# Kernel tuning notes

Hardware: AMD Instinct MI355X
Metric: run time of the kernel (lower is better)

Reference implementation:

```python
import jax, jax.numpy as jnp
import numpy as np

B, T = 32768, 32
OBJ_V, PRED_V = 179, 46
E_OBJ, E_PRED, H = 5, 5, 32
IN_DIM = E_OBJ + E_PRED + 2 + 4  # 16, matches LSTMCell input size


def setup_inputs() -> dict:
    key = jax.random.key(0)
    ks = jax.random.split(key, 12)
    s = 0.1
    return {
        "input_objects": jax.random.randint(ks[0], (B, T), 0, OBJ_V),
        "input_boxes": jax.random.uniform(ks[1], (B, T, 4), dtype=jnp.float32),
        "predicates": jax.random.randint(ks[2], (B, T), 0, PRED_V),
        "subject_indicators": jax.random.randint(ks[3], (B, T), 0, 2),
        "target_object": jax.random.randint(ks[4], (B,), 0, OBJ_V),
        "obj_emb": jax.random.normal(ks[5], (OBJ_V, E_OBJ), dtype=jnp.float32) * s,
        "pred_emb": jax.random.normal(ks[6], (PRED_V, E_PRED), dtype=jnp.float32) * s,
        "W_ih": jax.random.normal(ks[7], (4 * H, IN_DIM), dtype=jnp.float32) * s,
        "W_hh": jax.random.normal(ks[8], (4 * H, H), dtype=jnp.float32) * s,
        "b_ih": jnp.zeros((4 * H,), dtype=jnp.float32),
        "b_hh": jnp.zeros((4 * H,), dtype=jnp.float32),
        "fc2_W": jax.random.normal(ks[9], (4, H), dtype=jnp.float32) * s,
        "fc2_b": jnp.zeros((4,), dtype=jnp.float32),
    }


def _forward(input_objects, input_boxes, predicates, subject_indicators,
             obj_emb, pred_emb, W_ih, W_hh, b_ih, b_hh, fc2_W, fc2_b):
    # concatenate_features, vectorized over all timesteps at once: [B,T,16]
    feats = jnp.concatenate([
        obj_emb[input_objects],                                   # [B,T,5]
        pred_emb[predicates],                                     # [B,T,5]
        jax.nn.one_hot(subject_indicators, 2, dtype=jnp.float32), # [B,T,2]
        input_boxes,                                              # [B,T,4]
    ], axis=-1)
    xs = jnp.transpose(feats, (1, 0, 2))  # [T,B,16] for scan over time

    def step(carry, x):
        h, c = carry
        gates = x @ W_ih.T + b_ih + h @ W_hh.T + b_hh  # [B,4H]
        i, f, g, o = jnp.split(gates, 4, axis=-1)      # torch gate order i,f,g,o
        i = jax.nn.sigmoid(i)
        f = jax.nn.sigmoid(f)
        g = jnp.tanh(g)
        o = jax.nn.sigmoid(o)
        c = f * c + i * g
        h = o * jnp.tanh(c)
        return (h, c), None

    h0 = jnp.zeros((input_objects.shape[0], H), dtype=jnp.float32)
    (h, _), _ = jax.lax.scan(step, (h0, h0), xs)
    out = h @ fc2_W.T + fc2_b          # output_fc2 on last hidden state
    return jnp.clip(out, 0.0, 1.0)     # torch.clamp(min=0, max=1)


def reference(input_objects, input_boxes, predicates, subject_indicators, target_object,
              obj_emb, pred_emb, W_ih, W_hh, b_ih, b_hh, fc2_W, fc2_b):
    # target_object is accepted by the torch forward but unused in its body
    return _forward(input_objects, input_boxes, predicates, subject_indicators,
                    obj_emb, pred_emb, W_ih, W_hh, b_ih, b_hh, fc2_W, fc2_b)
```

## Files before the change

kernel.cpp:

```cpp
#include <hip/hip_runtime.h>

#define LDS_BYTES 16672

typedef _Float16 f16x8 __attribute__((ext_vector_type(8)));
typedef float    f32x4 __attribute__((ext_vector_type(4)));

#define LOG2E     1.44269504088896f
#define TWO_LOG2E 2.88539008177793f

__device__ __forceinline__ float sig_pre(float a) {
    return __builtin_amdgcn_rcpf(1.0f + __builtin_amdgcn_exp2f(a));
}
__device__ __forceinline__ float tanh_pre(float a) {
    return 1.0f - 2.0f * __builtin_amdgcn_rcpf(1.0f + __builtin_amdgcn_exp2f(a));
}
__device__ __forceinline__ int pack2(float a, float b) {
    union { _Float16 h[2]; int i; } u;
    u.h[0] = (_Float16)a; u.h[1] = (_Float16)b;
    return u.i;
}

__global__ __launch_bounds__(64, 2)
void lstm_fused(const int* __restrict__ objs,
                const float* __restrict__ boxes,
                const int* __restrict__ preds,
                const int* __restrict__ subj,
                const float* __restrict__ obj_emb,
                const float* __restrict__ pred_emb,
                const float* __restrict__ W_ih,
                const float* __restrict__ W_hh,
                const float* __restrict__ b_ih,
                const float* __restrict__ b_hh,
                const float* __restrict__ fc2_W,
                const float* __restrict__ fc2_b,
                float* __restrict__ out)
{
    extern __shared__ char smem[];
    const int tid  = threadIdx.x;
    const int quad = tid >> 4;
    const int cidx = tid & 15;
    const int XOFF = 0, ZOFF = 16640;

    if (tid < 8) ((int*)(smem + ZOFF))[tid] = 0;

    {
        int b  = tid >> 2;
        int t0 = (tid & 3) << 3;
        long gb = (long)blockIdx.x * 16 + b;
        const int* op = objs  + gb * 32 + t0;
        const int* pp = preds + gb * 32 + t0;
        const int* sp = subj  + gb * 32 + t0;
        #pragma unroll
        for (int c = 0; c < 8; c += 4) {
            int4 ov = *(const int4*)(op + c);
            int4 pv = *(const int4*)(pp + c);
            int4 sv = *(const int4*)(sp + c);
            int oarr[4] = {ov.x, ov.y, ov.z, ov.w};
            int parr[4] = {pv.x, pv.y, pv.z, pv.w};
            int sarr[4] = {sv.x, sv.y, sv.z, sv.w};
            #pragma unroll
            for (int tt = 0; tt < 4; ++tt) {
                int t = t0 + c + tt;
                const float* eo = obj_emb  + oarr[tt] * 5;
                const float* ep = pred_emb + parr[tt] * 5;
                float4 bx = *(const float4*)(boxes + (gb * 32 + t) * 4);
                f16x8 lo, hi;
                lo[0]=(_Float16)eo[0]; lo[1]=(_Float16)eo[1]; lo[2]=(_Float16)eo[2];
                lo[3]=(_Float16)eo[3]; lo[4]=(_Float16)eo[4];
                lo[5]=(_Float16)ep[0]; lo[6]=(_Float16)ep[1]; lo[7]=(_Float16)ep[2];
                hi[0]=(_Float16)ep[3]; hi[1]=(_Float16)ep[4];
                hi[2]=(_Float16)(sarr[tt]==0 ? 1.0f : 0.0f);
                hi[3]=(_Float16)(sarr[tt]==1 ? 1.0f : 0.0f);
                hi[4]=(_Float16)bx.x; hi[5]=(_Float16)bx.y;
                hi[6]=(_Float16)bx.z; hi[7]=(_Float16)bx.w;
                char* dst = smem + XOFF + b * 1040 + t * 32;
                *(f16x8*)dst        = lo;
                *(f16x8*)(dst + 16) = hi;
            }
        }
    }

    f16x8 Wf[8][2];
    f32x4 bias4[8];
    #pragma unroll
    for (int j = 0; j < 8; ++j) {
        int g = j >> 1, half = j & 1;
        float scale = (g == 2) ? TWO_LOG2E : -LOG2E;
        int um = 8 * (cidx >> 2) + (cidx & 3) + 4 * half;
        int n  = g * 32 + um;
        #pragma unroll
        for (int ks = 0; ks < 2; ++ks) {
            f16x8 v;
            #pragma unroll
            for (int jj = 0; jj < 8; ++jj) {
                int k = ks * 32 + quad * 8 + jj;
                float val = (k < 16) ? W_ih[n * 16 + k]
                          : (k >= 32) ? W_hh[n * 32 + (k - 32)]
                          : 0.0f;
                v[jj] = (_Float16)(val * scale);
            }
            Wf[j][ks] = v;
        }
        #pragma unroll
        for (int r = 0; r < 4; ++r) {
            int ur = 8 * quad + r + 4 * half;
            bias4[j][r] = (b_ih[g * 32 + ur] + b_hh[g * 32 + ur]) * scale;
        }
    }

    const bool qlow = (quad < 2);
    int       xaddr = qlow ? (XOFF + cidx * 1040 + quad * 16) : ZOFF;
    const int xinc  = qlow ? 32 : 0;

    __syncthreads();

    f16x8 xfrag = *(const f16x8*)(smem + xaddr); xaddr += xinc;
    f32x4 accp[8];
    #pragma unroll
    for (int j = 0; j < 8; ++j)
        accp[j] = __builtin_amdgcn_mfma_f32_16x16x32_f16(Wf[j][0], xfrag, bias4[j], 0, 0, 0);

    int pk0 = 0, pk1 = 0, pk2 = 0, pk3 = 0;
    float cst[8] = {0,0,0,0,0,0,0,0};
    float h_lo[4], h_hi[4];

    #pragma unroll 2
    for (int t = 0; t < 32; ++t) {
        union { int i[4]; f16x8 v; } hf;
        hf.i[0] = pk0; hf.i[1] = pk1; hf.i[2] = pk2; hf.i[3] = pk3;

        f32x4 acc[8];
        #pragma unroll
        for (int j = 0; j < 8; ++j)
            acc[j] = __builtin_amdgcn_mfma_f32_16x16x32_f16(Wf[j][1], hf.v, accp[j], 0, 0, 0);

        f16x8 xn = *(const f16x8*)(smem + xaddr); xaddr += xinc;

        #pragma unroll
        for (int r = 0; r < 4; ++r) {
            float i0 = sig_pre(acc[0][r]);
            float i1 = sig_pre(acc[1][r]);
            float f0 = sig_pre(acc[2][r]);
            float f1 = sig_pre(acc[3][r]);
            float g0 = tanh_pre(acc[4][r]);
            float g1 = tanh_pre(acc[5][r]);
            float o0 = sig_pre(acc[6][r]);
            float o1 = sig_pre(acc[7][r]);
            float c0 = fmaf(f0, cst[r],     i0 * g0);
            float c1 = fmaf(f1, cst[4 + r], i1 * g1);
            cst[r] = c0; cst[4 + r] = c1;
            h_lo[r] = o0 * tanh_pre(c0 * TWO_LOG2E);
            h_hi[r] = o1 * tanh_pre(c1 * TWO_LOG2E);
        }
        pk0 = pack2(h_lo[0], h_lo[1]);
        pk1 = pack2(h_lo[2], h_lo[3]);
        pk2 = pack2(h_hi[0], h_hi[1]);
        pk3 = pack2(h_hi[2], h_hi[3]);

        #pragma unroll
        for (int j = 0; j < 8; ++j)
            accp[j] = __builtin_amdgcn_mfma_f32_16x16x32_f16(Wf[j][0], xn, bias4[j], 0, 0, 0);
    }

    __syncthreads();
    #pragma unroll
    for (int r = 0; r < 4; ++r) {
        *(float*)(smem + cidx * 144 + (8 * quad + r) * 4)     = h_lo[r];
        *(float*)(smem + cidx * 144 + (8 * quad + 4 + r) * 4) = h_hi[r];
    }
    __syncthreads();

    {
        int b = tid >> 2, jj = tid & 3;
        const float* fw   = fc2_W + jj * 32;
        const float* hrow = (const float*)(smem + b * 144);
        float s = fc2_b[jj];
        #pragma unroll
        for (int k = 0; k < 8; ++k) {
            float4 hv = *(const float4*)(hrow + k * 4);
            s += fw[k*4+0] * hv.x + fw[k*4+1] * hv.y
               + fw[k*4+2] * hv.z + fw[k*4+3] * hv.w;
        }
        s = fminf(fmaxf(s, 0.0f), 1.0f);
        out[(long)blockIdx.x * 64 + tid] = s;
    }
}

extern "C" void kernel_launch(void* const* d_in, const int* in_sizes, int n_in,
                              void* d_out, int out_size, void* d_ws, size_t ws_size,
                              hipStream_t stream)
{
    lstm_fused<<<2048, 64, LDS_BYTES, stream>>>(
        (const int*)d_in[0], (const float*)d_in[1], (const int*)d_in[2],
        (const int*)d_in[3],
        (const float*)d_in[5], (const float*)d_in[6],
        (const float*)d_in[7], (const float*)d_in[8],
        (const float*)d_in[9], (const float*)d_in[10],
        (const float*)d_in[11], (const float*)d_in[12],
        (float*)d_out);
}
```

Measured before the change: 145.6 us.

## Split LSTM hidden units across two waves with LDS exchange of h per step

Each block now runs two wavefronts, each owning half of the hidden units (4 MFMAs per gate set instead of 8). After every timestep, each wave writes its packed half of h to a double-buffered LDS region and reads the other wave's half after a block barrier. The aim is to halve the per-wave serial MFMA and transcendental work on the recurrent critical path. The cost is a __syncthreads plus LDS round trip every step.

```diff
diff --git a/kernel.cpp b/kernel.cpp
--- a/kernel.cpp
+++ b/kernel.cpp
@@ -1,6 +1,6 @@
 #include <hip/hip_runtime.h>
 
-#define LDS_BYTES 16672
+#define LDS_BYTES 18720
 
 typedef _Float16 f16x8 __attribute__((ext_vector_type(8)));
 typedef float    f32x4 __attribute__((ext_vector_type(4)));
@@ -20,7 +20,7 @@
     return u.i;
 }
 
-__global__ __launch_bounds__(64, 2)
+__global__ __launch_bounds__(128, 4)
 void lstm_fused(const int* __restrict__ objs,
                 const float* __restrict__ boxes,
                 const int* __restrict__ preds,
@@ -37,56 +37,51 @@
 {
     extern __shared__ char smem[];
     const int tid  = threadIdx.x;
-    const int quad = tid >> 4;
-    const int cidx = tid & 15;
-    const int XOFF = 0, ZOFF = 16640;
+    const int lane = tid & 63;
+    const int wv   = tid >> 6;
+    const int quad = lane >> 4;
+    const int cidx = lane & 15;
+    const int XOFF = 0, HX0 = 16640, HX1 = 17664, ZOFF = 18688;
 
     if (tid < 8) ((int*)(smem + ZOFF))[tid] = 0;
 
     {
-        int b  = tid >> 2;
-        int t0 = (tid & 3) << 3;
+        int b  = tid >> 3;
+        int t0 = (tid & 7) << 2;
         long gb = (long)blockIdx.x * 16 + b;
-        const int* op = objs  + gb * 32 + t0;
-        const int* pp = preds + gb * 32 + t0;
-        const int* sp = subj  + gb * 32 + t0;
+        int4 ov = *(const int4*)(objs  + gb * 32 + t0);
+        int4 pv = *(const int4*)(preds + gb * 32 + t0);
+        int4 sv = *(const int4*)(subj  + gb * 32 + t0);
+        int oarr[4] = {ov.x, ov.y, ov.z, ov.w};
+        int parr[4] = {pv.x, pv.y, pv.z, pv.w};
+        int sarr[4] = {sv.x, sv.y, sv.z, sv.w};
         #pragma unroll
-        for (int c = 0; c < 8; c += 4) {
-            int4 ov = *(const int4*)(op + c);
-            int4 pv = *(const int4*)(pp + c);
-            int4 sv = *(const int4*)(sp + c);
-            int oarr[4] = {ov.x, ov.y, ov.z, ov.w};
-            int parr[4] = {pv.x, pv.y, pv.z, pv.w};
-            int sarr[4] = {sv.x, sv.y, sv.z, sv.w};
-            #pragma unroll
-            for (int tt = 0; tt < 4; ++tt) {
-                int t = t0 + c + tt;
-                const float* eo = obj_emb  + oarr[tt] * 5;
-                const float* ep = pred_emb + parr[tt] * 5;
-                float4 bx = *(const float4*)(boxes + (gb * 32 + t) * 4);
-                f16x8 lo, hi;
-                lo[0]=(_Float16)eo[0]; lo[1]=(_Float16)eo[1]; lo[2]=(_Float16)eo[2];
-                lo[3]=(_Float16)eo[3]; lo[4]=(_Float16)eo[4];
-                lo[5]=(_Float16)ep[0]; lo[6]=(_Float16)ep[1]; lo[7]=(_Float16)ep[2];
-                hi[0]=(_Float16)ep[3]; hi[1]=(_Float16)ep[4];
-                hi[2]=(_Float16)(sarr[tt]==0 ? 1.0f : 0.0f);
-                hi[3]=(_Float16)(sarr[tt]==1 ? 1.0f : 0.0f);
-                hi[4]=(_Float16)bx.x; hi[5]=(_Float16)bx.y;
-                hi[6]=(_Float16)bx.z; hi[7]=(_Float16)bx.w;
-                char* dst = smem + XOFF + b * 1040 + t * 32;
-                *(f16x8*)dst        = lo;
-                *(f16x8*)(dst + 16) = hi;
-            }
+        for (int tt = 0; tt < 4; ++tt) {
+            int t = t0 + tt;
+            const float* eo = obj_emb  + oarr[tt] * 5;
+            const float* ep = pred_emb + parr[tt] * 5;
+            float4 bx = *(const float4*)(boxes + (gb * 32 + t) * 4);
+            f16x8 lo, hi;
+            lo[0]=(_Float16)eo[0]; lo[1]=(_Float16)eo[1]; lo[2]=(_Float16)eo[2];
+            lo[3]=(_Float16)eo[3]; lo[4]=(_Float16)eo[4];
+            lo[5]=(_Float16)ep[0]; lo[6]=(_Float16)ep[1]; lo[7]=(_Float16)ep[2];
+            hi[0]=(_Float16)ep[3]; hi[1]=(_Float16)ep[4];
+            hi[2]=(_Float16)(sarr[tt]==0 ? 1.0f : 0.0f);
+            hi[3]=(_Float16)(sarr[tt]==1 ? 1.0f : 0.0f);
+            hi[4]=(_Float16)bx.x; hi[5]=(_Float16)bx.y;
+            hi[6]=(_Float16)bx.z; hi[7]=(_Float16)bx.w;
+            char* dst = smem + XOFF + b * 1040 + t * 32;
+            *(f16x8*)dst        = lo;
+            *(f16x8*)(dst + 16) = hi;
         }
     }
 
-    f16x8 Wf[8][2];
-    f32x4 bias4[8];
+    f16x8 Wf[4][2];
+    f32x4 bias4[4];
     #pragma unroll
-    for (int j = 0; j < 8; ++j) {
-        int g = j >> 1, half = j & 1;
+    for (int g = 0; g < 4; ++g) {
         float scale = (g == 2) ? TWO_LOG2E : -LOG2E;
-        int um = 8 * (cidx >> 2) + (cidx & 3) + 4 * half;
+        int um = 8 * (cidx >> 2) + (cidx & 3) + 4 * wv;
         int n  = g * 32 + um;
         #pragma unroll
         for (int ks = 0; ks < 2; ++ks) {
@@ -99,78 +94,81 @@
                           : 0.0f;
                 v[jj] = (_Float16)(val * scale);
             }
-            Wf[j][ks] = v;
+            Wf[g][ks] = v;
         }
         #pragma unroll
         for (int r = 0; r < 4; ++r) {
-            int ur = 8 * quad + r + 4 * half;
-            bias4[j][r] = (b_ih[g * 32 + ur] + b_hh[g * 32 + ur]) * scale;
+            int ur = 8 * quad + 4 * wv + r;
+            bias4[g][r] = (b_ih[g * 32 + ur] + b_hh[g * 32 + ur]) * scale;
         }
     }
 
     const bool qlow = (quad < 2);
     int       xaddr = qlow ? (XOFF + cidx * 1040 + quad * 16) : ZOFF;
     const int xinc  = qlow ? 32 : 0;
+    const int wr_off = wv * 512 + lane * 8;
+    const int rd_off = (1 - wv) * 512 + lane * 8;
 
     __syncthreads();
 
     f16x8 xfrag = *(const f16x8*)(smem + xaddr); xaddr += xinc;
-    f32x4 accp[8];
+    f32x4 accp[4];
     #pragma unroll
-    for (int j = 0; j < 8; ++j)
-        accp[j] = __builtin_amdgcn_mfma_f32_16x16x32_f16(Wf[j][0], xfrag, bias4[j], 0, 0, 0);
+    for (int g = 0; g < 4; ++g)
+        accp[g] = __builtin_amdgcn_mfma_f32_16x16x32_f16(Wf[g][0], xfrag, bias4[g], 0, 0, 0);
 
-    int pk0 = 0, pk1 = 0, pk2 = 0, pk3 = 0;
-    float cst[8] = {0,0,0,0,0,0,0,0};
-    float h_lo[4], h_hi[4];
+    int pk0 = 0, pk1 = 0;
+    int rd0 = 0, rd1 = 0;
+    float cst[4] = {0,0,0,0};
+    float hr[4];
 
     #pragma unroll 2
     for (int t = 0; t < 32; ++t) {
         union { int i[4]; f16x8 v; } hf;
-        hf.i[0] = pk0; hf.i[1] = pk1; hf.i[2] = pk2; hf.i[3] = pk3;
+        hf.i[0] = wv ? rd0 : pk0;
+        hf.i[1] = wv ? rd1 : pk1;
+        hf.i[2] = wv ? pk0 : rd0;
+        hf.i[3] = wv ? pk1 : rd1;
 
-        f32x4 acc[8];
+        f32x4 acc[4];
         #pragma unroll
-        for (int j = 0; j < 8; ++j)
-            acc[j] = __builtin_amdgcn_mfma_f32_16x16x32_f16(Wf[j][1], hf.v, accp[j], 0, 0, 0);
+        for (int g = 0; g < 4; ++g)
+            acc[g] = __builtin_amdgcn_mfma_f32_16x16x32_f16(Wf[g][1], hf.v, accp[g], 0, 0, 0);
 
         f16x8 xn = *(const f16x8*)(smem + xaddr); xaddr += xinc;
 
         #pragma unroll
         for (int r = 0; r < 4; ++r) {
-            float i0 = sig_pre(acc[0][r]);
-            float i1 = sig_pre(acc[1][r]);
-            float f0 = sig_pre(acc[2][r]);
-            float f1 = sig_pre(acc[3][r]);
-            float g0 = tanh_pre(acc[4][r]);
-            float g1 = tanh_pre(acc[5][r]);
-            float o0 = sig_pre(acc[6][r]);
-            float o1 = sig_pre(acc[7][r]);
-            float c0 = fmaf(f0, cst[r],     i0 * g0);
-            float c1 = fmaf(f1, cst[4 + r], i1 * g1);
-            cst[r] = c0; cst[4 + r] = c1;
-            h_lo[r] = o0 * tanh_pre(c0 * TWO_LOG2E);
-            h_hi[r] = o1 * tanh_pre(c1 * TWO_LOG2E);
+            float iv = sig_pre(acc[0][r]);
+            float fv = sig_pre(acc[1][r]);
+            float gv = tanh_pre(acc[2][r]);
+            float ov = sig_pre(acc[3][r]);
+            float c  = fmaf(fv, cst[r], iv * gv);
+            cst[r] = c;
+            hr[r] = ov * tanh_pre(c * TWO_LOG2E);
         }
-        pk0 = pack2(h_lo[0], h_lo[1]);
-        pk1 = pack2(h_lo[2], h_lo[3]);
-        pk2 = pack2(h_hi[0], h_hi[1]);
-        pk3 = pack2(h_hi[2], h_hi[3]);
+        pk0 = pack2(hr[0], hr[1]);
+        pk1 = pack2(hr[2], hr[3]);
+
+        char* buf = smem + ((t & 1) ? HX1 : HX0);
+        *(int2*)(buf + wr_off) = (int2){pk0, pk1};
 
         #pragma unroll
-        for (int j = 0; j < 8; ++j)
-            accp[j] = __builtin_amdgcn_mfma_f32_16x16x32_f16(Wf[j][0], xn, bias4[j], 0, 0, 0);
+        for (int g = 0; g < 4; ++g)
+            accp[g] = __builtin_amdgcn_mfma_f32_16x16x32_f16(Wf[g][0], xn, bias4[g], 0, 0, 0);
+
+        __syncthreads();
+        int2 rd = *(const int2*)(buf + rd_off);
+        rd0 = rd.x; rd1 = rd.y;
     }
 
     __syncthreads();
     #pragma unroll
-    for (int r = 0; r < 4; ++r) {
-        *(float*)(smem + cidx * 144 + (8 * quad + r) * 4)     = h_lo[r];
-        *(float*)(smem + cidx * 144 + (8 * quad + 4 + r) * 4) = h_hi[r];
-    }
+    for (int r = 0; r < 4; ++r)
+        *(float*)(smem + cidx * 144 + (8 * quad + 4 * wv + r) * 4) = hr[r];
     __syncthreads();
 
-    {
+    if (tid < 64) {
         int b = tid >> 2, jj = tid & 3;
         const float* fw   = fc2_W + jj * 32;
         const float* hrow = (const float*)(smem + b * 144);
@@ -190,7 +188,7 @@
                               void* d_out, int out_size, void* d_ws, size_t ws_size,
                               hipStream_t stream)
 {
-    lstm_fused<<<2048, 64, LDS_BYTES, stream>>>(
+    lstm_fused<<<2048, 128, LDS_BYTES, stream>>>(
         (const int*)d_in[0], (const float*)d_in[1], (const int*)d_in[2],
         (const int*)d_in[3],
         (const float*)d_in[5], (const float*)d_in[6],
```

Result: no change. 143.6 us (-1.4%).

## Interleave two independent batch chunks per wave and fuse LSTM gate reciprocals

Applied to the files above, without the earlier changes.

Each 64-thread block now handles 32 sequences as two interleaved 16-row chunks. This gives the recurrent loop two independent MFMA and transcendental dependency chains to hide latency, and the grid is halved. The gate math is rewritten algebraically so the cell update needs one reciprocal instead of several sigmoid/tanh reciprocals per element. It costs more registers and LDS, and the launch bound drops to one wave occupancy hint, which lowers the number of resident waves.

```diff
diff --git a/kernel.cpp b/kernel.cpp
--- a/kernel.cpp
+++ b/kernel.cpp
@@ -1,6 +1,6 @@
 #include <hip/hip_runtime.h>
 
-#define LDS_BYTES 16672
+#define LDS_BYTES 33328
 
 typedef _Float16 f16x8 __attribute__((ext_vector_type(8)));
 typedef float    f32x4 __attribute__((ext_vector_type(4)));
@@ -8,19 +8,13 @@
 #define LOG2E     1.44269504088896f
 #define TWO_LOG2E 2.88539008177793f
 
-__device__ __forceinline__ float sig_pre(float a) {
-    return __builtin_amdgcn_rcpf(1.0f + __builtin_amdgcn_exp2f(a));
-}
-__device__ __forceinline__ float tanh_pre(float a) {
-    return 1.0f - 2.0f * __builtin_amdgcn_rcpf(1.0f + __builtin_amdgcn_exp2f(a));
-}
 __device__ __forceinline__ int pack2(float a, float b) {
     union { _Float16 h[2]; int i; } u;
     u.h[0] = (_Float16)a; u.h[1] = (_Float16)b;
     return u.i;
 }
 
-__global__ __launch_bounds__(64, 2)
+__global__ __launch_bounds__(64, 1)
 void lstm_fused(const int* __restrict__ objs,
                 const float* __restrict__ boxes,
                 const int* __restrict__ preds,
@@ -39,28 +33,31 @@
     const int tid  = threadIdx.x;
     const int quad = tid >> 4;
     const int cidx = tid & 15;
-    const int XOFF = 0, ZOFF = 16640;
-
-    if (tid < 8) ((int*)(smem + ZOFF))[tid] = 0;
+    const int ZOFF = 33280;
+
+    if (tid < 12) ((int*)(smem + ZOFF))[tid] = 0;
 
     {
-        int b  = tid >> 2;
-        int t0 = (tid & 3) << 3;
-        long gb = (long)blockIdx.x * 16 + b;
+        int row = tid >> 1;
+        int ch  = row >> 4;
+        int b   = row & 15;
+        int t0  = (tid & 1) << 4;
+        long gb = (long)blockIdx.x * 32 + row;
         const int* op = objs  + gb * 32 + t0;
         const int* pp = preds + gb * 32 + t0;
         const int* sp = subj  + gb * 32 + t0;
-        #pragma unroll
-        for (int c = 0; c < 8; c += 4) {
-            int4 ov = *(const int4*)(op + c);
-            int4 pv = *(const int4*)(pp + c);
-            int4 sv = *(const int4*)(sp + c);
+        char* base = smem + ch * 16640 + b * 1040;
+        #pragma unroll
+        for (int c4 = 0; c4 < 16; c4 += 4) {
+            int4 ov = *(const int4*)(op + c4);
+            int4 pv = *(const int4*)(pp + c4);
+            int4 sv = *(const int4*)(sp + c4);
             int oarr[4] = {ov.x, ov.y, ov.z, ov.w};
             int parr[4] = {pv.x, pv.y, pv.z, pv.w};
             int sarr[4] = {sv.x, sv.y, sv.z, sv.w};
             #pragma unroll
             for (int tt = 0; tt < 4; ++tt) {
-                int t = t0 + c + tt;
+                int t = t0 + c4 + tt;
                 const float* eo = obj_emb  + oarr[tt] * 5;
                 const float* ep = pred_emb + parr[tt] * 5;
                 float4 bx = *(const float4*)(boxes + (gb * 32 + t) * 4);
@@ -73,7 +70,7 @@
                 hi[3]=(_Float16)(sarr[tt]==1 ? 1.0f : 0.0f);
                 hi[4]=(_Float16)bx.x; hi[5]=(_Float16)bx.y;
                 hi[6]=(_Float16)bx.z; hi[7]=(_Float16)bx.w;
-                char* dst = smem + XOFF + b * 1040 + t * 32;
+                char* dst = base + t * 32;
                 *(f16x8*)dst        = lo;
                 *(f16x8*)(dst + 16) = hi;
             }
@@ -109,80 +106,115 @@
     }
 
     const bool qlow = (quad < 2);
-    int       xaddr = qlow ? (XOFF + cidx * 1040 + quad * 16) : ZOFF;
-    const int xinc  = qlow ? 32 : 0;
+    int xaddr[2];
+    xaddr[0] = qlow ? (0     + cidx * 1040 + quad * 16) : ZOFF;
+    xaddr[1] = qlow ? (16640 + cidx * 1040 + quad * 16) : ZOFF;
+    const int xinc = qlow ? 32 : 0;
 
     __syncthreads();
 
-    f16x8 xfrag = *(const f16x8*)(smem + xaddr); xaddr += xinc;
-    f32x4 accp[8];
+    f32x4 accp[2][8];
     #pragma unroll
-    for (int j = 0; j < 8; ++j)
-        accp[j] = __builtin_amdgcn_mfma_f32_16x16x32_f16(Wf[j][0], xfrag, bias4[j], 0, 0, 0);
-
-    int pk0 = 0, pk1 = 0, pk2 = 0, pk3 = 0;
-    float cst[8] = {0,0,0,0,0,0,0,0};
-    float h_lo[4], h_hi[4];
-
-    #pragma unroll 2
+    for (int ch = 0; ch < 2; ++ch) {
+        f16x8 xf = *(const f16x8*)(smem + xaddr[ch]); xaddr[ch] += xinc;
+        #pragma unroll
+        for (int j = 0; j < 8; ++j)
+            accp[ch][j] = __builtin_amdgcn_mfma_f32_16x16x32_f16(Wf[j][0], xf, bias4[j], 0, 0, 0);
+    }
+
+    int   pk[2][4] = {{0,0,0,0},{0,0,0,0}};
+    float cst[2][8] = {{0,0,0,0,0,0,0,0},{0,0,0,0,0,0,0,0}};
+    float hlo[2][4], hhi[2][4];
+
     for (int t = 0; t < 32; ++t) {
-        union { int i[4]; f16x8 v; } hf;
-        hf.i[0] = pk0; hf.i[1] = pk1; hf.i[2] = pk2; hf.i[3] = pk3;
-
-        f32x4 acc[8];
+        f32x4 acc[2][8];
+        #pragma unroll
+        for (int ch = 0; ch < 2; ++ch) {
+            union { int i[4]; f16x8 v; } hf;
+            hf.i[0] = pk[ch][0]; hf.i[1] = pk[ch][1];
+            hf.i[2] = pk[ch][2]; hf.i[3] = pk[ch][3];
+            #pragma unroll
+            for (int j = 0; j < 8; ++j)
+                acc[ch][j] = __builtin_amdgcn_mfma_f32_16x16x32_f16(Wf[j][1], hf.v, accp[ch][j], 0, 0, 0);
+        }
+
+        f16x8 xn0 = *(const f16x8*)(smem + xaddr[0]); xaddr[0] += xinc;
+        f16x8 xn1 = *(const f16x8*)(smem + xaddr[1]); xaddr[1] += xinc;
+
+        #pragma unroll
+        for (int ch = 0; ch < 2; ++ch) {
+            #pragma unroll
+            for (int r = 0; r < 4; ++r) {
+                float Ei0 = __builtin_amdgcn_exp2f(acc[ch][0][r]);
+                float Ei1 = __builtin_amdgcn_exp2f(acc[ch][1][r]);
+                float Ef0 = __builtin_amdgcn_exp2f(acc[ch][2][r]);
+                float Ef1 = __builtin_amdgcn_exp2f(acc[ch][3][r]);
+                float Eg0 = __builtin_amdgcn_exp2f(acc[ch][4][r]);
+                float Eg1 = __builtin_amdgcn_exp2f(acc[ch][5][r]);
+                float Eo0 = __builtin_amdgcn_exp2f(acc[ch][6][r]);
+                float Eo1 = __builtin_amdgcn_exp2f(acc[ch][7][r]);
+
+                float t10  = 1.0f + Ei0;
+                float t11  = 1.0f + Ei1;
+                float dig0 = fmaf(t10, Eg0, t10);
+                float dig1 = fmaf(t11, Eg1, t11);
+                float tf0  = 1.0f + Ef0;
+                float tf1  = 1.0f + Ef1;
+                float n0   = fmaf(Eg0 - 1.0f, tf0, cst[ch][r]     * dig0);
+                float n1   = fmaf(Eg1 - 1.0f, tf1, cst[ch][4 + r] * dig1);
+                float c0   = n0 * __builtin_amdgcn_rcpf(tf0 * dig0);
+                float c1   = n1 * __builtin_amdgcn_rcpf(tf1 * dig1);
+                cst[ch][r] = c0; cst[ch][4 + r] = c1;
+                float Ec0  = __builtin_amdgcn_exp2f(c0 * TWO_LOG2E);
+                float Ec1  = __builtin_amdgcn_exp2f(c1 * TWO_LOG2E);
+                float to0  = 1.0f + Eo0;
+                float to1  = 1.0f + Eo1;
+                float dh0  = fmaf(to0, Ec0, to0);
+                float dh1  = fmaf(to1, Ec1, to1);
+                hlo[ch][r] = (Ec0 - 1.0f) * __builtin_amdgcn_rcpf(dh0);
+                hhi[ch][r] = (Ec1 - 1.0f) * __builtin_amdgcn_rcpf(dh1);
+            }
+            pk[ch][0] = pack2(hlo[ch][0], hlo[ch][1]);
+            pk[ch][1] = pack2(hlo[ch][2], hlo[ch][3]);
+            pk[ch][2] = pack2(hhi[ch][0], hhi[ch][1]);
+            pk[ch][3] = pack2(hhi[ch][2], hhi[ch][3]);
+        }
+
         #pragma unroll
         for (int j = 0; j < 8; ++j)
-            acc[j] = __builtin_amdgcn_mfma_f32_16x16x32_f16(Wf[j][1], hf.v, accp[j], 0, 0, 0);
-
-        f16x8 xn = *(const f16x8*)(smem + xaddr); xaddr += xinc;
-
-        #pragma unroll
-        for (int r = 0; r < 4; ++r) {
-            float i0 = sig_pre(acc[0][r]);
-            float i1 = sig_pre(acc[1][r]);
-            float f0 = sig_pre(acc[2][r]);
-            float f1 = sig_pre(acc[3][r]);
-            float g0 = tanh_pre(acc[4][r]);
-            float g1 = tanh_pre(acc[5][r]);
-            float o0 = sig_pre(acc[6][r]);
-            float o1 = sig_pre(acc[7][r]);
-            float c0 = fmaf(f0, cst[r],     i0 * g0);
-            float c1 = fmaf(f1, cst[4 + r], i1 * g1);
-            cst[r] = c0; cst[4 + r] = c1;
-            h_lo[r] = o0 * tanh_pre(c0 * TWO_LOG2E);
-            h_hi[r] = o1 * tanh_pre(c1 * TWO_LOG2E);
-        }
-        pk0 = pack2(h_lo[0], h_lo[1]);
-        pk1 = pack2(h_lo[2], h_lo[3]);
-        pk2 = pack2(h_hi[0], h_hi[1]);
-        pk3 = pack2(h_hi[2], h_hi[3]);
-
+            accp[0][j] = __builtin_amdgcn_mfma_f32_16x16x32_f16(Wf[j][0], xn0, bias4[j], 0, 0, 0);
         #pragma unroll
         for (int j = 0; j < 8; ++j)
-            accp[j] = __builtin_amdgcn_mfma_f32_16x16x32_f16(Wf[j][0], xn, bias4[j], 0, 0, 0);
+            accp[1][j] = __builtin_amdgcn_mfma_f32_16x16x32_f16(Wf[j][0], xn1, bias4[j], 0, 0, 0);
     }
 
     __syncthreads();
     #pragma unroll
-    for (int r = 0; r < 4; ++r) {
-        *(float*)(smem + cidx * 144 + (8 * quad + r) * 4)     = h_lo[r];
-        *(float*)(smem + cidx * 144 + (8 * quad + 4 + r) * 4) = h_hi[r];
-    }
+    for (int ch = 0; ch < 2; ++ch)
+        #pragma unroll
+        for (int r = 0; r < 4; ++r) {
+            *(float*)(smem + ch * 2304 + cidx * 144 + (8 * quad + r) * 4)     = hlo[ch][r];
+            *(float*)(smem + ch * 2304 + cidx * 144 + (8 * quad + 4 + r) * 4) = hhi[ch][r];
+        }
     __syncthreads();
 
     {
         int b = tid >> 2, jj = tid & 3;
-        const float* fw   = fc2_W + jj * 32;
-        const float* hrow = (const float*)(smem + b * 144);
-        float s = fc2_b[jj];
-        #pragma unroll
-        for (int k = 0; k < 8; ++k) {
-            float4 hv = *(const float4*)(hrow + k * 4);
-            s += fw[k*4+0] * hv.x + fw[k*4+1] * hv.y
-               + fw[k*4+2] * hv.z + fw[k*4+3] * hv.w;
-        }
-        s = fminf(fmaxf(s, 0.0f), 1.0f);
-        out[(long)blockIdx.x * 64 + tid] = s;
+        const float* fw = fc2_W + jj * 32;
+        float fb = fc2_b[jj];
+        #pragma unroll
+        for (int ch = 0; ch < 2; ++ch) {
+            const float* hrow = (const float*)(smem + ch * 2304 + b * 144);
+            float s = fb;
+            #pragma unroll
+            for (int k = 0; k < 8; ++k) {
+                float4 hv = *(const float4*)(hrow + k * 4);
+                s += fw[k*4+0] * hv.x + fw[k*4+1] * hv.y
+                   + fw[k*4+2] * hv.z + fw[k*4+3] * hv.w;
+            }
+            s = fminf(fmaxf(s, 0.0f), 1.0f);
+            out[(long)blockIdx.x * 128 + ch * 64 + tid] = s;
+        }
     }
 }
 
@@ -190,7 +222,7 @@
                               void* d_out, int out_size, void* d_ws, size_t ws_size,
                               hipStream_t stream)
 {
-    lstm_fused<<<2048, 64, LDS_BYTES, stream>>>(
+    lstm_fused<<<1024, 64, LDS_BYTES, stream>>>(
         (const int*)d_in[0], (const float*)d_in[1], (const int*)d_in[2],
         (const int*)d_in[3],
         (const float*)d_in[5], (const float*)d_in[6],
```

New measurement: 146.6 us. No clear change (+0.7%).
